# Performance work log

Hardware: AMD Instinct MI355X
Metric: run time of the kernel (lower is better)

## Reference

```python
import jax, jax.numpy as jnp
import numpy as np

NEG_INF = -9.0e15  # matches torch's -9000000000000000.0 mask value
ALPHA = 0.2        # LeakyReLU negative slope


def setup_inputs() -> dict:
    key = jax.random.key(0)
    k1, k2, k3, k4 = jax.random.split(key, 4)
    N, F_in, F_out = 8192, 128, 128
    x = jax.random.normal(k1, (N, F_in), dtype=jnp.float32)
    adj = jax.random.randint(k2, (N, N), 0, 2, dtype=jnp.int32)
    W = jax.random.normal(k3, (F_in, F_out), dtype=jnp.float32) * (1.0 / np.sqrt(F_in))
    a = jax.random.normal(k4, (2 * F_out, 1), dtype=jnp.float32) * (1.0 / np.sqrt(2 * F_out))
    return {"x": x, "adj": adj, "W": W, "a": a}


def reference(x, adj, W, a):
    # h = W(input): [N, F_out]
    h = x @ W
    F_out = h.shape[1]
    # a([h_i || h_j]) = h_i . a[:F] + h_j . a[F:]  -- identical math to the
    # original NxNx2F concat, without materializing it.
    a_src = a[:F_out, 0]   # coefficients on the row (i) node
    a_dst = a[F_out:, 0]   # coefficients on the column (j) node
    s_src = h @ a_src      # [N]
    s_dst = h @ a_dst      # [N]
    e = jax.nn.leaky_relu(s_src[:, None] + s_dst[None, :], negative_slope=ALPHA)  # [N, N]
    e = jnp.where(adj > 0, e, jnp.float32(NEG_INF))
    attention = jax.nn.softmax(e, axis=1)
    # dropout omitted (identity at eval) for a deterministic baseline
    h_prime = attention @ h  # [N, F_out]
    return h_prime
```

## Files before the change

### kernel.cpp

```cpp
#include <hip/hip_runtime.h>

#define N 8192
#define F 128
#define NS 8
#define JC (N / NS)
#define CK 32
#define NC (JC / CK)
#define ALPHA 0.2f

typedef __attribute__((ext_vector_type(8))) short short8;
typedef __attribute__((ext_vector_type(4))) float f32x4;
typedef unsigned short u16;

__device__ __forceinline__ u16 f2bf(float f) {
    unsigned int u = __float_as_uint(f);
    u += 0x7fff + ((u >> 16) & 1);
    return (u16)(u >> 16);
}
__device__ __forceinline__ float bf2f(u16 b) {
    return __uint_as_float(((unsigned int)b) << 16);
}
__device__ __forceinline__ float lrelu(float z) { return fmaxf(z, ALPHA * z); }

__global__ __launch_bounds__(256) void gemm_h(const float* __restrict__ x,
                                              const float* __restrict__ W,
                                              const float* __restrict__ aa,
                                              u16* __restrict__ hT,
                                              float* __restrict__ ssrc,
                                              float* __restrict__ sdst) {
    __shared__ float xs[32 * 128];
    __shared__ float Wsh[32 * 128];
    const int t = threadIdx.x;
    const int i0 = blockIdx.x * 32;
    const int c4 = (t & 31) * 4;
    const int r8 = t >> 5;

#pragma unroll
    for (int p = 0; p < 4; ++p) {
        int rr = p * 8 + r8;
        *(float4*)&xs[rr * 128 + c4] = *(const float4*)&x[(size_t)(i0 + rr) * 128 + c4];
    }

    const int tx = t & 31, ty = t >> 5;
    const int r0 = ty * 4, c0 = tx * 4;
    float acc[4][4] = {};

    for (int kc = 0; kc < 4; ++kc) {
        __syncthreads();
#pragma unroll
        for (int p = 0; p < 4; ++p) {
            int k = p * 8 + r8;
            *(float4*)&Wsh[k * 128 + c4] = *(const float4*)&W[(kc * 32 + k) * 128 + c4];
        }
        __syncthreads();
#pragma unroll 4
        for (int k = 0; k < 32; k += 4) {
            float xr[4][4];
#pragma unroll
            for (int rr = 0; rr < 4; ++rr)
                *(float4*)xr[rr] = *(const float4*)&xs[(r0 + rr) * 128 + kc * 32 + k];
#pragma unroll
            for (int kk = 0; kk < 4; ++kk) {
                float4 wv = *(const float4*)&Wsh[(k + kk) * 128 + c0];
#pragma unroll
                for (int rr = 0; rr < 4; ++rr) {
                    acc[rr][0] += xr[rr][kk] * wv.x;
                    acc[rr][1] += xr[rr][kk] * wv.y;
                    acc[rr][2] += xr[rr][kk] * wv.z;
                    acc[rr][3] += xr[rr][kk] * wv.w;
                }
            }
        }
    }

#pragma unroll
    for (int rr = 0; rr < 4; ++rr)
#pragma unroll
        for (int cc = 0; cc < 4; ++cc)
            hT[(size_t)(c0 + cc) * N + (i0 + r0 + rr)] = f2bf(acc[rr][cc]);

    float4 asv = *(const float4*)&aa[c0];
    float4 adv = *(const float4*)&aa[F + c0];
#pragma unroll
    for (int rr = 0; rr < 4; ++rr) {
        float vs = acc[rr][0] * asv.x + acc[rr][1] * asv.y + acc[rr][2] * asv.z + acc[rr][3] * asv.w;
        float vd = acc[rr][0] * adv.x + acc[rr][1] * adv.y + acc[rr][2] * adv.z + acc[rr][3] * adv.w;
#pragma unroll
        for (int off = 16; off >= 1; off >>= 1) {
            vs += __shfl_down(vs, off, 32);
            vd += __shfl_down(vd, off, 32);
        }
        if (tx == 0) {
            ssrc[i0 + r0 + rr] = vs;
            sdst[i0 + r0 + rr] = vd;
        }
    }
}

__global__ __launch_bounds__(256, 4) void attn_mfma(const int* __restrict__ adj,
                                                    const u16* __restrict__ hT,
                                                    const float* __restrict__ ssrc,
                                                    const float* __restrict__ sdst,
                                                    float* __restrict__ pacc,
                                                    float* __restrict__ pS) {
    const int t = threadIdx.x;
    const int w = t >> 6, L = t & 63;
    const int quad = L >> 4, l16 = L & 15;
    const int i0 = blockIdx.x * 64 + w * 16;
    const int split = blockIdx.y;
    const int jbase = split * JC;

    const int row = i0 + l16;
    const float s_i = ssrc[row];
    const int* pA = adj + (size_t)row * N + jbase + quad * 8;
    const float* pD = sdst + jbase + quad * 8;
    const u16* pB = hT + (size_t)l16 * N + jbase + quad * 8;

    f32x4 acc[8];
#pragma unroll
    for (int cg = 0; cg < 8; ++cg) acc[cg] = 0.f;
    float rsum = 0.f;

    int4 aj[2][2];
    float4 sd[2][2];
    aj[0][0] = *(const int4*)(pA);
    aj[0][1] = *(const int4*)(pA + 4);
    sd[0][0] = *(const float4*)(pD);
    sd[0][1] = *(const float4*)(pD + 4);
    aj[1][0] = *(const int4*)(pA + CK);
    aj[1][1] = *(const int4*)(pA + CK + 4);
    sd[1][0] = *(const float4*)(pD + CK);
    sd[1][1] = *(const float4*)(pD + CK + 4);

#pragma unroll 2
    for (int c = 0; c < NC; ++c) {
        const int s = c & 1;
        const int off = c * CK;

        short8 B0[4];
#pragma unroll
        for (int cg = 0; cg < 4; ++cg)
            B0[cg] = *(const short8*)(pB + (size_t)cg * 16 * N + off);

        short8 wf;
        {
            int m[8] = {aj[s][0].x, aj[s][0].y, aj[s][0].z, aj[s][0].w,
                        aj[s][1].x, aj[s][1].y, aj[s][1].z, aj[s][1].w};
            float d[8] = {sd[s][0].x, sd[s][0].y, sd[s][0].z, sd[s][0].w,
                          sd[s][1].x, sd[s][1].y, sd[s][1].z, sd[s][1].w};
#pragma unroll
            for (int k = 0; k < 8; ++k) {
                float e = __expf(lrelu(s_i + d[k]));
                float wv = (m[k] > 0) ? e : 0.f;
                u16 b = f2bf(wv);
                rsum += bf2f(b);
                wf[k] = (short)b;
            }
        }

        const int cp = (c + 2 < NC) ? c + 2 : c;
        const int offp = cp * CK;
        aj[s][0] = *(const int4*)(pA + offp);
        aj[s][1] = *(const int4*)(pA + offp + 4);
        sd[s][0] = *(const float4*)(pD + offp);
        sd[s][1] = *(const float4*)(pD + offp + 4);

        short8 B1[4];
#pragma unroll
        for (int cg = 0; cg < 4; ++cg)
            B1[cg] = *(const short8*)(pB + (size_t)(cg + 4) * 16 * N + off);

#pragma unroll
        for (int cg = 0; cg < 4; ++cg)
            acc[cg] = __builtin_amdgcn_mfma_f32_16x16x32_bf16(wf, B0[cg], acc[cg], 0, 0, 0);
#pragma unroll
        for (int cg = 0; cg < 4; ++cg)
            acc[cg + 4] = __builtin_amdgcn_mfma_f32_16x16x32_bf16(wf, B1[cg], acc[cg + 4], 0, 0, 0);
    }

    float* dst = pacc + (size_t)split * N * F;
#pragma unroll
    for (int cg = 0; cg < 8; ++cg) {
        const int col = cg * 16 + l16;
        const int r0 = i0 + quad * 4;
#pragma unroll
        for (int r = 0; r < 4; ++r)
            dst[(size_t)(r0 + r) * F + col] = acc[cg][r];
    }

    rsum += __shfl_xor(rsum, 16);
    rsum += __shfl_xor(rsum, 32);
    if (L < 16) pS[(size_t)split * N + i0 + l16] = rsum;
}

__global__ __launch_bounds__(256) void finalize(float* __restrict__ out,
                                                const float* __restrict__ pacc,
                                                const float* __restrict__ pS) {
    const int idx = (blockIdx.x * 256 + threadIdx.x) * 4;
    const int i = idx >> 7;
    float s = 0.f;
#pragma unroll
    for (int k = 0; k < NS; ++k) s += pS[(size_t)k * N + i];
    float4 a = {0.f, 0.f, 0.f, 0.f};
#pragma unroll
    for (int k = 0; k < NS; ++k) {
        float4 v = *(const float4*)&pacc[(size_t)k * N * F + idx];
        a.x += v.x; a.y += v.y; a.z += v.z; a.w += v.w;
    }
    const float inv = 1.0f / s;
    float4 o = {a.x * inv, a.y * inv, a.z * inv, a.w * inv};
    *(float4*)&out[idx] = o;
}

extern "C" void kernel_launch(void* const* d_in, const int* in_sizes, int n_in,
                              void* d_out, int out_size, void* d_ws, size_t ws_size,
                              hipStream_t stream) {
    (void)in_sizes; (void)n_in; (void)out_size; (void)ws_size;
    const float* x   = (const float*)d_in[0];
    const int*   adj = (const int*)d_in[1];
    const float* W   = (const float*)d_in[2];
    const float* a   = (const float*)d_in[3];
    float* out = (float*)d_out;

    u16* hT     = (u16*)d_ws;
    float* ssrc = (float*)(hT + (size_t)N * F);
    float* sdst = ssrc + N;
    float* pS   = sdst + N;
    float* pacc = pS + (size_t)NS * N;

    gemm_h<<<N / 32, 256, 0, stream>>>(x, W, a, hT, ssrc, sdst);
    attn_mfma<<<dim3(N / 64, NS), 256, 0, stream>>>(adj, hT, ssrc, sdst, pacc, pS);
    finalize<<<(N * F / 4) / 256, 256, 0, stream>>>(out, pacc, pS);
}
```

Baseline: 509.2 us.

## Stage hT tiles in LDS via async DMA and share attention weights across waves

The attention kernel now copies hT column tiles into double-buffered, XOR-swizzled shared memory with global_load_lds, and writes the bf16 attention weights for a 32-row block into LDS. Waves then split the 128 output features instead of each re-reading all of hT from global memory. The row-tile size, j-chunk size and split count change (NS 8 to 4). This is meant to cut redundant global and L2 traffic on hT. In exchange it adds two __syncthreads per chunk and more LDS use, which may lower occupancy.

```diff
diff --git a/kernel.cpp b/kernel.cpp
--- a/kernel.cpp
+++ b/kernel.cpp
@@ -2,10 +2,12 @@
 
 #define N 8192
 #define F 128
-#define NS 8
-#define JC (N / NS)
-#define CK 32
-#define NC (JC / CK)
+#define NS 4
+#define JT (N / NS)
+#define CJ 64
+#define NC (JT / CJ)
+#define TI 32
+#define WT_STRIDE 72
 #define ALPHA 0.2f
 
 typedef __attribute__((ext_vector_type(8))) short short8;
@@ -21,6 +23,11 @@
     return __uint_as_float(((unsigned int)b) << 16);
 }
 __device__ __forceinline__ float lrelu(float z) { return fmaxf(z, ALPHA * z); }
+
+__device__ __forceinline__ void dma16(const void* g, void* l) {
+    __builtin_amdgcn_global_load_lds((__attribute__((address_space(1))) void*)g,
+                                     (__attribute__((address_space(3))) void*)l, 16, 0, 0);
+}
 
 __global__ __launch_bounds__(256) void gemm_h(const float* __restrict__ x,
                                               const float* __restrict__ W,
@@ -103,94 +110,112 @@
                                                     const float* __restrict__ sdst,
                                                     float* __restrict__ pacc,
                                                     float* __restrict__ pS) {
+    __shared__ u16 bt[2][128 * CJ];
+    __shared__ u16 wt[TI * WT_STRIDE];
+
     const int t = threadIdx.x;
     const int w = t >> 6, L = t & 63;
     const int quad = L >> 4, l16 = L & 15;
-    const int i0 = blockIdx.x * 64 + w * 16;
+    const int i0 = blockIdx.x * TI;
     const int split = blockIdx.y;
-    const int jbase = split * JC;
-
-    const int row = i0 + l16;
-    const float s_i = ssrc[row];
-    const int* pA = adj + (size_t)row * N + jbase + quad * 8;
-    const float* pD = sdst + jbase + quad * 8;
-    const u16* pB = hT + (size_t)l16 * N + jbase + quad * 8;
-
-    f32x4 acc[8];
-#pragma unroll
-    for (int cg = 0; cg < 8; ++cg) acc[cg] = 0.f;
-    float rsum = 0.f;
-
-    int4 aj[2][2];
-    float4 sd[2][2];
-    aj[0][0] = *(const int4*)(pA);
-    aj[0][1] = *(const int4*)(pA + 4);
-    sd[0][0] = *(const float4*)(pD);
-    sd[0][1] = *(const float4*)(pD + 4);
-    aj[1][0] = *(const int4*)(pA + CK);
-    aj[1][1] = *(const int4*)(pA + CK + 4);
-    sd[1][0] = *(const float4*)(pD + CK);
-    sd[1][1] = *(const float4*)(pD + CK + 4);
-
-#pragma unroll 2
+    const int j0 = split * JT;
+
+    const int ar = t >> 4;
+    const int ac = (t & 15) * 4;
+    const float s_i0 = ssrc[i0 + ar];
+    const float s_i1 = ssrc[i0 + 16 + ar];
+    const size_t arow0 = (size_t)(i0 + ar) * N;
+    const size_t arow1 = (size_t)(i0 + 16 + ar) * N;
+
+    const int bf = t >> 3;
+    const int bsj = (t & 7) ^ (bf & 7);
+    const size_t bgoff = (size_t)bf * N + j0 + bsj * 8;
+
+    const int rt = w & 1;
+    const int colbase = (w >> 1) * 4;
+
+    f32x4 acc[4];
+#pragma unroll
+    for (int ci = 0; ci < 4; ++ci) acc[ci] = 0.f;
+    float sum0 = 0.f, sum1 = 0.f;
+
+#pragma unroll
+    for (int rp = 0; rp < 4; ++rp)
+        dma16(hT + bgoff + (size_t)rp * 32 * N, &bt[0][rp * 2048 + w * 512]);
+    int4 a0 = *(const int4*)(adj + arow0 + j0 + ac);
+    int4 a1 = *(const int4*)(adj + arow1 + j0 + ac);
+    float4 dv = *(const float4*)(sdst + j0 + ac);
+
     for (int c = 0; c < NC; ++c) {
-        const int s = c & 1;
-        const int off = c * CK;
-
-        short8 B0[4];
-#pragma unroll
-        for (int cg = 0; cg < 4; ++cg)
-            B0[cg] = *(const short8*)(pB + (size_t)cg * 16 * N + off);
-
-        short8 wf;
+        ushort4 wlo, whi;
         {
-            int m[8] = {aj[s][0].x, aj[s][0].y, aj[s][0].z, aj[s][0].w,
-                        aj[s][1].x, aj[s][1].y, aj[s][1].z, aj[s][1].w};
-            float d[8] = {sd[s][0].x, sd[s][0].y, sd[s][0].z, sd[s][0].w,
-                          sd[s][1].x, sd[s][1].y, sd[s][1].z, sd[s][1].w};
-#pragma unroll
-            for (int k = 0; k < 8; ++k) {
-                float e = __expf(lrelu(s_i + d[k]));
-                float wv = (m[k] > 0) ? e : 0.f;
-                u16 b = f2bf(wv);
-                rsum += bf2f(b);
-                wf[k] = (short)b;
+            int m0[4] = {a0.x, a0.y, a0.z, a0.w};
+            int m1[4] = {a1.x, a1.y, a1.z, a1.w};
+            float d[4] = {dv.x, dv.y, dv.z, dv.w};
+            u16 q0[4], q1[4];
+#pragma unroll
+            for (int k = 0; k < 4; ++k) {
+                float e0 = __expf(lrelu(s_i0 + d[k]));
+                float e1 = __expf(lrelu(s_i1 + d[k]));
+                q0[k] = f2bf(m0[k] > 0 ? e0 : 0.f);
+                q1[k] = f2bf(m1[k] > 0 ? e1 : 0.f);
+                sum0 += bf2f(q0[k]);
+                sum1 += bf2f(q1[k]);
             }
-        }
-
-        const int cp = (c + 2 < NC) ? c + 2 : c;
-        const int offp = cp * CK;
-        aj[s][0] = *(const int4*)(pA + offp);
-        aj[s][1] = *(const int4*)(pA + offp + 4);
-        sd[s][0] = *(const float4*)(pD + offp);
-        sd[s][1] = *(const float4*)(pD + offp + 4);
-
-        short8 B1[4];
-#pragma unroll
-        for (int cg = 0; cg < 4; ++cg)
-            B1[cg] = *(const short8*)(pB + (size_t)(cg + 4) * 16 * N + off);
-
-#pragma unroll
-        for (int cg = 0; cg < 4; ++cg)
-            acc[cg] = __builtin_amdgcn_mfma_f32_16x16x32_bf16(wf, B0[cg], acc[cg], 0, 0, 0);
-#pragma unroll
-        for (int cg = 0; cg < 4; ++cg)
-            acc[cg + 4] = __builtin_amdgcn_mfma_f32_16x16x32_bf16(wf, B1[cg], acc[cg + 4], 0, 0, 0);
+            wlo = {q0[0], q0[1], q0[2], q0[3]};
+            whi = {q1[0], q1[1], q1[2], q1[3]};
+        }
+
+        __syncthreads();
+        *(ushort4*)&wt[ar * WT_STRIDE + ac] = wlo;
+        *(ushort4*)&wt[(16 + ar) * WT_STRIDE + ac] = whi;
+        __syncthreads();
+
+        const int cn = (c + 1 < NC) ? c + 1 : c;
+        const size_t jn = (size_t)cn * CJ;
+        {
+            u16* dstb = bt[(c + 1) & 1];
+#pragma unroll
+            for (int rp = 0; rp < 4; ++rp)
+                dma16(hT + bgoff + (size_t)rp * 32 * N + jn, &dstb[rp * 2048 + w * 512]);
+        }
+        a0 = *(const int4*)(adj + arow0 + j0 + jn + ac);
+        a1 = *(const int4*)(adj + arow1 + j0 + jn + ac);
+        dv = *(const float4*)(sdst + j0 + jn + ac);
+
+        const u16* btc = bt[c & 1];
+#pragma unroll
+        for (int ks = 0; ks < 2; ++ks) {
+            short8 A = *(const short8*)&wt[(rt * 16 + l16) * WT_STRIDE + ks * 32 + quad * 8];
+#pragma unroll
+            for (int ci = 0; ci < 4; ++ci) {
+                const int f = (colbase + ci) * 16 + l16;
+                const int s = (ks * 4 + quad) ^ (f & 7);
+                short8 B = *(const short8*)&btc[(f >> 5) * 2048 + (f & 31) * 64 + s * 8];
+                acc[ci] = __builtin_amdgcn_mfma_f32_16x16x32_bf16(A, B, acc[ci], 0, 0, 0);
+            }
+        }
     }
 
     float* dst = pacc + (size_t)split * N * F;
 #pragma unroll
-    for (int cg = 0; cg < 8; ++cg) {
-        const int col = cg * 16 + l16;
-        const int r0 = i0 + quad * 4;
+    for (int ci = 0; ci < 4; ++ci) {
+        const int col = (colbase + ci) * 16 + l16;
+        const int r0 = i0 + rt * 16 + quad * 4;
 #pragma unroll
         for (int r = 0; r < 4; ++r)
-            dst[(size_t)(r0 + r) * F + col] = acc[cg][r];
-    }
-
-    rsum += __shfl_xor(rsum, 16);
-    rsum += __shfl_xor(rsum, 32);
-    if (L < 16) pS[(size_t)split * N + i0 + l16] = rsum;
+            dst[(size_t)(r0 + r) * F + col] = acc[ci][r];
+    }
+
+#pragma unroll
+    for (int off = 8; off >= 1; off >>= 1) {
+        sum0 += __shfl_down(sum0, off, 16);
+        sum1 += __shfl_down(sum1, off, 16);
+    }
+    if ((t & 15) == 0) {
+        pS[(size_t)split * N + i0 + ar] = sum0;
+        pS[(size_t)split * N + i0 + 16 + ar] = sum1;
+    }
 }
 
 __global__ __launch_bounds__(256) void finalize(float* __restrict__ out,
@@ -229,6 +254,6 @@
     float* pacc = pS + (size_t)NS * N;
 
     gemm_h<<<N / 32, 256, 0, stream>>>(x, W, a, hT, ssrc, sdst);
-    attn_mfma<<<dim3(N / 64, NS), 256, 0, stream>>>(adj, hT, ssrc, sdst, pacc, pS);
+    attn_mfma<<<dim3(N / TI, NS), 256, 0, stream>>>(adj, hT, ssrc, sdst, pacc, pS);
     finalize<<<(N * F / 4) / 256, 256, 0, stream>>>(out, pacc, pS);
 }
```

After: 414.8 us. 1.23x faster.
